# Kernel tuning notes

Measured on AMD Instinct MI355X. Metric: run time of the kernel, lower is better.

Reference implementation:

```python
import jax, jax.numpy as jnp
import numpy as np

DIM = 256
N_EMBED = 1024


def setup_inputs() -> dict:
    key = jax.random.key(0)
    k1, k2, k3 = jax.random.split(key, 3)
    input_hr = jax.random.normal(k1, (8, 64, 64, DIM), dtype=jnp.float32)
    input_lr = jax.random.normal(k2, (8, 64, 64, DIM), dtype=jnp.float32)
    # original init: uniform_(-1/n_embed, -1/n_embed) is a constant; use small uniform noise
    # around it so argmin is non-degenerate while staying faithful in scale.
    embed_lr = -1.0 / N_EMBED + 0.01 * jax.random.uniform(k3, (DIM, N_EMBED), dtype=jnp.float32)
    return {"input_hr": input_hr, "input_lr": input_lr, "embed_lr": embed_lr}


def _nearest(flat, embed):
    # flat: [N, D], embed: [D, K]
    dist = (flat ** 2).sum(1, keepdims=True) - 2.0 * flat @ embed + (embed ** 2).sum(0, keepdims=True)  # [N, K]
    ind = jnp.argmax(-dist, axis=1)  # [N]
    quant = embed.T[ind]  # [N, D]  (== F.embedding(ind, embed.T))
    return dist, ind, quant


def reference(input_hr, input_lr, embed_lr):
    shp = input_hr.shape
    flat_hr = input_hr.reshape(-1, DIM)
    flat_lr = input_lr.reshape(-1, DIM)

    # LC and HC paths use the identical codebook (embed_lr) in the original module,
    # so the distances/indices/quantized values are numerically identical; compute once.
    dist_hr, ind_hr, q_hr = _nearest(flat_hr, embed_lr)
    dist_lr, ind_lr, q_lr = _nearest(flat_lr, embed_lr)

    q_hr = q_hr.reshape(shp)
    q_lr = q_lr.reshape(shp)
    ind_hr = ind_hr.reshape(shp[:-1])
    ind_lr = ind_lr.reshape(shp[:-1])

    # eval mode (code_book_opt=False): diff = mean((quantize.detach() - input)^2)
    diff_hr = jnp.mean((jax.lax.stop_gradient(q_hr) - input_hr) ** 2)
    diff_lr = jnp.mean((jax.lax.stop_gradient(q_lr) - input_lr) ** 2)

    # straight-through estimator
    ste_hr = input_hr + jax.lax.stop_gradient(q_hr - input_hr)
    ste_lr = input_lr + jax.lax.stop_gradient(q_lr - input_lr)

    return (ste_hr, ste_lr, ste_hr, ste_lr,
            diff_hr, diff_lr, diff_hr, diff_lr,
            ind_hr, ind_lr, ind_hr, ind_lr,
            dist_hr, dist_lr, dist_hr, dist_lr)
```

## Files before the change

kernel.cpp:

```cpp
#include <hip/hip_runtime.h>
#include <stdint.h>

typedef _Float16 half8 __attribute__((ext_vector_type(8)));
typedef float f32x4 __attribute__((ext_vector_type(4)));

#define MARGIN 1e-3f

#define O_STE_HR1 0
#define O_STE_LR1 8388608
#define O_STE_HR2 16777216
#define O_STE_LR2 25165824
#define O_DIFF    33554432
#define O_IND_HR1 33554436
#define O_IND_LR1 33587204
#define O_IND_HR2 33619972
#define O_IND_LR2 33652740
#define O_DIST_HR1 33685508
#define O_DIST_LR1 67239940
#define O_DIST_HR2 100794372
#define O_DIST_LR2 134348804

#define CNT_U32_OFF 4194304

#define W_DIFF 0
#define W_CNT  16
#define W_SSE  4096
#define W_EF16 8192
#define W_ET   532480
#define W_FIND     7872512
#define W_FROWS    8134656
#define W_FMIN     8396800
#define W_T1       8658944
#define W_T3       8921088

__device__ __forceinline__ void ins2(unsigned long long k, unsigned long long &a, unsigned long long &b){
  if (k < a){ b = a; a = k; } else if (k < b){ b = k; }
}

__global__ __launch_bounds__(256) void prep(const float* __restrict__ e, char* __restrict__ ws){
  __shared__ float tile[64][65];
  int t = threadIdx.x;
  int k0 = (blockIdx.x & 3) * 64;
  int c0 = (blockIdx.x >> 2) * 64;
  float* Et = (float*)(ws + W_ET);
  _Float16* Ef = (_Float16*)(ws + W_EF16);
  float* sse = (float*)(ws + W_SSE);
#pragma unroll
  for (int p = 0; p < 4; p++){
    int kr = p*16 + (t >> 4);
    int cc = (t & 15) * 4;
    float4 v = *(const float4*)(e + (k0 + kr)*1024 + c0 + cc);
    tile[kr][cc+0]=v.x; tile[kr][cc+1]=v.y; tile[kr][cc+2]=v.z; tile[kr][cc+3]=v.w;
  }
  __syncthreads();
#pragma unroll
  for (int p = 0; p < 4; p++){
    int cr = p*16 + (t >> 4);
    int kc = (t & 15) * 4;
    float4 v;
    v.x = tile[kc+0][cr]; v.y = tile[kc+1][cr]; v.z = tile[kc+2][cr]; v.w = tile[kc+3][cr];
    *(float4*)(Et + (c0+cr)*256 + k0 + kc) = v;
    union { _Float16 h[4]; unsigned long long u; } pk;
    pk.h[0]=(_Float16)v.x; pk.h[1]=(_Float16)v.y; pk.h[2]=(_Float16)v.z; pk.h[3]=(_Float16)v.w;
    *(unsigned long long*)(Ef + (c0+cr)*256 + k0 + kc) = pk.u;
  }
  if (t < 64){
    float s = 0.f;
    for (int k = 0; k < 64; k++){ float v = tile[k][t]; s += v*v; }
    atomicAdd(&sse[c0 + t], s);
  }
}

__global__ __launch_bounds__(256) void t1x_np(const float* __restrict__ xhr, const float* __restrict__ xlr,
                                              char* __restrict__ ws, float* __restrict__ out){
  __shared__ float rowbuf[64][260];
  int b = blockIdx.x;
  int h = b >> 9;
  int r0 = (b & 511) * 64;
  const float* X = h ? xlr : xhr;
  _Float16* D = (_Float16*)(out + O_DIST_HR2) + (size_t)h*8388608;
  int t = threadIdx.x;
#pragma unroll
  for (int p = 0; p < 16; p++){
    int idx = p*256 + t;
    int rr = idx >> 6, cc = idx & 63;
    float4 v = *(const float4*)(X + (size_t)(r0+rr)*256 + cc*4);
    rowbuf[rr][cc*4+0]=v.x; rowbuf[rr][cc*4+1]=v.y; rowbuf[rr][cc*4+2]=v.z; rowbuf[rr][cc*4+3]=v.w;
    union { _Float16 h4[4]; unsigned long long u; } pk;
    pk.h4[0]=(_Float16)v.x; pk.h4[1]=(_Float16)v.y; pk.h4[2]=(_Float16)v.z; pk.h4[3]=(_Float16)v.w;
    *(unsigned long long*)(D + (size_t)(r0+rr)*256 + cc*4) = pk.u;
  }
  __syncthreads();
  if (t < 64){
    const float* a = &rowbuf[t][0];
    float blk[2];
#pragma unroll
    for (int p = 0; p < 2; p++){
      const float* ap = a + p*128;
      float s[16];
#pragma unroll
      for (int l = 0; l < 16; l++){
        float q0 = __fmul_rn(ap[l      ], ap[l      ]);
        float q1 = __fmul_rn(ap[l + 16 ], ap[l + 16 ]);
        float q2 = __fmul_rn(ap[l + 32 ], ap[l + 32 ]);
        float q3 = __fmul_rn(ap[l + 48 ], ap[l + 48 ]);
        float q4 = __fmul_rn(ap[l + 64 ], ap[l + 64 ]);
        float q5 = __fmul_rn(ap[l + 80 ], ap[l + 80 ]);
        float q6 = __fmul_rn(ap[l + 96 ], ap[l + 96 ]);
        float q7 = __fmul_rn(ap[l + 112], ap[l + 112]);
        s[l] = __fadd_rn(__fadd_rn(__fadd_rn(q0,q1), __fadd_rn(q2,q3)),
                         __fadd_rn(__fadd_rn(q4,q5), __fadd_rn(q6,q7)));
      }
      float u[8];
#pragma unroll
      for (int l = 0; l < 8; l++) u[l] = __fadd_rn(s[l], s[l+8]);
      float v[4];
#pragma unroll
      for (int l = 0; l < 4; l++) v[l] = __fadd_rn(u[l], u[l+4]);
      blk[p] = __fadd_rn(__fadd_rn(v[0], v[2]), __fadd_rn(v[1], v[3]));
    }
    ((float*)(ws + W_T1))[h*32768 + r0 + t] = __fadd_rn(blk[0], blk[1]);
  }
}

__global__ __launch_bounds__(256) void t3_np(const float* __restrict__ e, char* __restrict__ ws){
  int k = blockIdx.x*256 + threadIdx.x;
  float v0 = e[k];
  float acc = __fmul_rn(v0, v0);
  for (int i = 1; i < 256; i++){
    float v = e[i*1024 + k];
    acc = __fadd_rn(acc, __fmul_rn(v, v));
  }
  ((float*)(ws + W_T3))[k] = acc;
}

__global__ __launch_bounds__(512, 4) void gemm_dist(char* __restrict__ ws, float* __restrict__ out){
  __shared__ __align__(16) char smem[77312];
  _Float16* Bimg = (_Float16*)smem;
  float* sx = (float*)(smem + 65536);
  float* se = (float*)(smem + 66560);
  unsigned* f1tu = (unsigned*)(smem + 67072);
  unsigned* cntL = (unsigned*)(smem + 68096);
  unsigned long long* listL = (unsigned long long*)(smem + 69120);

  int bid = blockIdx.x;
  int xcd = bid & 7, slot = bid >> 3;
  int ct = slot & 7;
  int panel = ((slot >> 3) << 3) + xcd;
  int lrow0 = (panel & 127) << 8;
  int col0 = ct << 7;
  int t = threadIdx.x, lane = t & 63, wid = t >> 6;
  int wm = wid >> 1, wn = wid & 1;
  int kg = lane >> 4, rl = lane & 15;

  const _Float16* Xf = (const _Float16*)(out + O_DIST_HR2)
                     + ((panel < 128) ? 0 : 8388608) + (size_t)lrow0*256;

  const _Float16* Ef = (const _Float16*)(ws + W_EF16);
#pragma unroll
  for (int i = 0; i < 8; i++){
    int chunk = i*512 + t;
    int c = chunk >> 5, kc = chunk & 31;
    uint4 v = *(const uint4*)(Ef + (size_t)(col0 + c)*256 + kc*8);
    int off = c*512 + ((kc*16) ^ ((c & 7) << 4));
    *(uint4*)((char*)Bimg + off) = v;
  }
  if (t < 128) se[t] = ((const float*)(ws + W_SSE))[col0 + t];
  if (t < 256){
    sx[t] = ((const float*)(ws + W_T1))[((panel < 128) ? 0 : 32768) + lrow0 + t];
    f1tu[t] = 0xFFFFFFFFu;
    cntL[t] = 0u;
    listL[t*4+0] = ~0ull; listL[t*4+1] = ~0ull; listL[t*4+2] = ~0ull; listL[t*4+3] = ~0ull;
  }
  __syncthreads();

  f32x4 acc[4][4] = {};
#pragma unroll 2
  for (int kk = 0; kk < 8; kk++){
    half8 av[4], bv[4];
#pragma unroll
    for (int fm = 0; fm < 4; fm++){
      int row = wm*64 + fm*16 + rl;
      av[fm] = *(const half8*)(Xf + (size_t)row*256 + kk*32 + kg*8);
    }
#pragma unroll
    for (int fn = 0; fn < 4; fn++){
      int col = wn*64 + fn*16 + rl;
      bv[fn] = *(const half8*)((char*)Bimg + col*512 + ((kk*64 + kg*16) ^ ((col & 7) << 4)));
    }
#pragma unroll
    for (int fm = 0; fm < 4; fm++)
#pragma unroll
      for (int fn = 0; fn < 4; fn++)
        acc[fm][fn] = __builtin_amdgcn_mfma_f32_16x16x32_f16(av[fm], bv[fn], acc[fm][fn], 0, 0, 0);
  }
  __syncthreads();

  for (int fm = 0; fm < 4; fm++){
    float dmn[4] = {1e30f, 1e30f, 1e30f, 1e30f};
#pragma unroll
    for (int fn = 0; fn < 4; fn++){
      float sec = se[wn*64 + fn*16 + rl];
      f32x4 a = acc[fm][fn];
#pragma unroll
      for (int j = 0; j < 4; j++){
        int br = wm*64 + fm*16 + kg*4 + j;
        dmn[j] = fminf(dmn[j], fmaf(-2.f, a[j], sx[br] + sec));
      }
    }
#pragma unroll
    for (int m = 1; m < 16; m <<= 1)
#pragma unroll
      for (int j = 0; j < 4; j++)
        dmn[j] = fminf(dmn[j], __shfl_xor(dmn[j], m));
    if (rl == 0){
#pragma unroll
      for (int j = 0; j < 4; j++){
        int br = wm*64 + fm*16 + kg*4 + j;
        atomicMin(&f1tu[br], __float_as_uint(dmn[j]));
      }
    }
  }
  __syncthreads();

  for (int fm = 0; fm < 4; fm++){
#pragma unroll
    for (int j = 0; j < 4; j++){
      int br = wm*64 + fm*16 + kg*4 + j;
      float thrA = __uint_as_float(f1tu[br]) + MARGIN;
      float sxb = sx[br];
#pragma unroll
      for (int fn = 0; fn < 4; fn++){
        int col = wn*64 + fn*16 + rl;
        float d = fmaf(-2.f, acc[fm][fn][j], sxb + se[col]);
        *(_Float16*)(smem + br*256 + ((col*2) ^ ((br & 7) << 4))) = (_Float16)d;
        if (d <= thrA){
          unsigned idx = atomicAdd(&cntL[br], 1u);
          if (idx < 4u)
            listL[br*4 + idx] = ((unsigned long long)__float_as_uint(d) << 32) | (unsigned)(col0 + col);
        }
      }
    }
  }
  __syncthreads();

  size_t growbase = (size_t)(((panel < 128) ? 0 : 32768) + lrow0);
  char* stg = (char*)out;
#pragma unroll
  for (int it = 0; it < 16; it++){
    int idx = it*512 + t;
    int row = idx >> 5, c8 = idx & 31;
    unsigned long long v = *(const unsigned long long*)(smem + row*256 + ((c8*8) ^ ((row & 7) << 4)));
    __builtin_nontemporal_store(v,
      (unsigned long long*)(stg + (growbase + row)*2048 + col0*2 + c8*8));
  }

  if (t < 256){
    int rc = panel*256 + t;
    unsigned long long* KO = (unsigned long long*)(out + O_DIST_HR1);
    size_t kb = ((size_t)rc*8 + (size_t)ct)*4;
    KO[kb+0] = listL[t*4+0]; KO[kb+1] = listL[t*4+1];
    KO[kb+2] = listL[t*4+2]; KO[kb+3] = listL[t*4+3];
    ((unsigned*)(out + O_DIST_HR1))[CNT_U32_OFF + rc*8 + ct] = cntL[t];
  }
}

__global__ __launch_bounds__(256) void merge_flag(char* __restrict__ ws, const float* __restrict__ out){
  int rc = blockIdx.x*256 + threadIdx.x;
  const unsigned long long* K = (const unsigned long long*)(out + O_DIST_HR1);
  const unsigned* C = (const unsigned*)(out + O_DIST_HR1) + CNT_U32_OFF;
  unsigned long long a = ~0ull, b = ~0ull;
  bool ovf = false;
#pragma unroll
  for (int ct = 0; ct < 8; ct++){
    ovf = ovf || (C[(size_t)rc*8 + ct] > 4u);
    size_t base = ((size_t)rc*8 + (size_t)ct)*4;
#pragma unroll
    for (int q = 0; q < 4; q++) ins2(K[base+q], a, b);
  }
  ((int*)(ws + W_FIND))[rc] = (int)(unsigned)(a & 0xFFFFFFFFu);
  float f1 = __uint_as_float((unsigned)(a >> 32));
  float f2 = __uint_as_float((unsigned)(b >> 32));
  if (ovf || (f2 - f1 < MARGIN)){
    unsigned idx = atomicAdd((unsigned*)(ws + W_CNT), 1u);
    ((int*)(ws + W_FROWS))[idx] = rc | (ovf ? (int)0x80000000 : 0);
    ((float*)(ws + W_FMIN))[idx] = f1;
  }
}

__device__ __forceinline__ float exact_d(const float4* __restrict__ x4, const float* __restrict__ Et,
                                         float t1v, const float* __restrict__ T3, int k){
  const float4* e4 = (const float4*)(Et + (size_t)k*256);
  float c = 0.f;
  for (int i = 0; i < 64; i++){
    float4 xv = x4[i], ev = e4[i];
    c = fmaf(xv.x, ev.x, c);
    c = fmaf(xv.y, ev.y, c);
    c = fmaf(xv.z, ev.z, c);
    c = fmaf(xv.w, ev.w, c);
  }
  return __fadd_rn(__fsub_rn(t1v, __fmul_rn(2.f, c)), T3[k]);
}

__global__ __launch_bounds__(256) void refine_np(const float* __restrict__ xhr, const float* __restrict__ xlr,
                                                 char* __restrict__ ws, const float* __restrict__ out){
  unsigned nf = *(const unsigned*)(ws + W_CNT);
  int lane = threadIdx.x & 63;
  unsigned wgl = blockIdx.x*4 + (threadIdx.x >> 6);
  const float* Et = (const float*)(ws + W_ET);
  const float* T1 = (const float*)(ws + W_T1);
  const float* T3 = (const float*)(ws + W_T3);
  const int* rows = (const int*)(ws + W_FROWS);
  const float* fmn = (const float*)(ws + W_FMIN);
  int* find = (int*)(ws + W_FIND);
  const unsigned long long* K = (const unsigned long long*)(out + O_DIST_HR1);
  for (unsigned ii = wgl; ii < nf; ii += gridDim.x*4){
    int rcw = rows[ii];
    bool ovf = rcw < 0;
    int rc = rcw & 0x7FFFFFFF;
    int h = rc >> 15, r = rc & 32767;
    const float4* x4 = (const float4*)((h ? xlr : xhr) + (size_t)r*256);
    float t1v = T1[rc];
    unsigned long long bestkey = ~0ull;
    if (!ovf){
      if (lane < 32){
        unsigned long long kk = K[(size_t)rc*32 + lane];
        float dm = __uint_as_float((unsigned)(kk >> 32));
        if (dm <= fmn[ii] + MARGIN){
          int k = (int)(unsigned)(kk & 0xFFFFFFFFu);
          float d = exact_d(x4, Et, t1v, T3, k);
          bestkey = ((unsigned long long)__float_as_uint(d) << 32) | (unsigned)k;
        }
      }
    } else {
      for (int k = lane; k < 1024; k += 64){
        float d = exact_d(x4, Et, t1v, T3, k);
        unsigned long long key = ((unsigned long long)__float_as_uint(d) << 32) | (unsigned)k;
        if (key < bestkey) bestkey = key;
      }
    }
#pragma unroll
    for (int m2 = 1; m2 < 64; m2 <<= 1){
      unsigned long long o = __shfl_xor(bestkey, m2);
      if (o < bestkey) bestkey = o;
    }
    if (lane == 0) find[rc] = (int)(unsigned)(bestkey & 0xFFFFFFFFu);
  }
}

__global__ __launch_bounds__(256) void expand_dist(float* __restrict__ out){
  const unsigned long long* src = (const unsigned long long*)out;
  float* d1 = out + O_DIST_HR1;
  float* d2 = out + O_DIST_HR2;
  size_t i = (size_t)blockIdx.x*256 + threadIdx.x;
#pragma unroll
  for (int k = 0; k < 16; k++){
    size_t idx = (size_t)k*1048576 + i;
    union { unsigned long long u; _Float16 h[4]; } pk;
    pk.u = src[idx];
    f32x4 q;
    q[0] = (float)pk.h[0]; q[1] = (float)pk.h[1]; q[2] = (float)pk.h[2]; q[3] = (float)pk.h[3];
    __builtin_nontemporal_store(q, (f32x4*)(d1 + idx*4));
    __builtin_nontemporal_store(q, (f32x4*)(d2 + idx*4));
  }
}

__global__ __launch_bounds__(256) void finalize(const float* __restrict__ xhr, const float* __restrict__ xlr,
                                                char* __restrict__ ws, float* __restrict__ out){
  int b = blockIdx.x;
  int h = b >> 9, chunk = b & 511;
  const float* X = h ? xlr : xhr;
  int wid = threadIdx.x >> 6, lane = threadIdx.x & 63;
  const float* Et = (const float*)(ws + W_ET);
  const int* find = (const int*)(ws + W_FIND);
  int sb1 = h ? O_STE_LR1 : O_STE_HR1;
  int sb2 = h ? O_STE_LR2 : O_STE_HR2;
  int ib1 = h ? O_IND_LR1 : O_IND_HR1;
  int ib2 = h ? O_IND_LR2 : O_IND_HR2;
  double part = 0.0;
  for (int rr = wid; rr < 64; rr += 4){
    int r = chunk*64 + rr;
    int k = find[h*32768 + r];
    f32x4 q = *(const f32x4*)(Et + (size_t)k*256 + lane*4);
    f32x4 x = *(const f32x4*)(X + (size_t)r*256 + lane*4);
    __builtin_nontemporal_store(q, (f32x4*)(out + sb1 + r*256 + lane*4));
    __builtin_nontemporal_store(q, (f32x4*)(out + sb2 + r*256 + lane*4));
    if (lane == 0){ out[ib1 + r] = (float)k; out[ib2 + r] = (float)k; }
    double d0 = (double)q[0] - x[0], d1 = (double)q[1] - x[1];
    double d2 = (double)q[2] - x[2], d3 = (double)q[3] - x[3];
    part += d0*d0 + d1*d1 + d2*d2 + d3*d3;
  }
#pragma unroll
  for (int m = 1; m < 64; m <<= 1) part += __shfl_xor(part, m);
  __shared__ double wsum[4];
  if (lane == 0) wsum[wid] = part;
  __syncthreads();
  if (threadIdx.x == 0)
    atomicAdd((double*)(ws + W_DIFF) + h, wsum[0] + wsum[1] + wsum[2] + wsum[3]);
}

__global__ void fin_diff(const char* __restrict__ ws, float* __restrict__ out){
  if (threadIdx.x == 0 && blockIdx.x == 0){
    const double* d = (const double*)(ws + W_DIFF);
    float dh = (float)(d[0] / 8388608.0);
    float dl = (float)(d[1] / 8388608.0);
    out[O_DIFF+0] = dh; out[O_DIFF+1] = dl; out[O_DIFF+2] = dh; out[O_DIFF+3] = dl;
  }
}

extern "C" void kernel_launch(void* const* d_in, const int* in_sizes, int n_in,
                              void* d_out, int out_size, void* d_ws, size_t ws_size,
                              hipStream_t stream){
  const float* xhr = (const float*)d_in[0];
  const float* xlr = (const float*)d_in[1];
  const float* emb = (const float*)d_in[2];
  float* out = (float*)d_out;
  char* ws = (char*)d_ws;
  hipMemsetAsync(d_ws, 0, 8192, stream);
  prep<<<64, 256, 0, stream>>>(emb, ws);
  t1x_np<<<1024, 256, 0, stream>>>(xhr, xlr, ws, out);
  t3_np<<<4, 256, 0, stream>>>(emb, ws);
  gemm_dist<<<2048, 512, 0, stream>>>(ws, out);
  merge_flag<<<256, 256, 0, stream>>>(ws, out);
  refine_np<<<2048, 256, 0, stream>>>(xhr, xlr, ws, out);
  expand_dist<<<4096, 256, 0, stream>>>(out);
  finalize<<<1024, 256, 0, stream>>>(xhr, xlr, ws, out);
  fin_diff<<<1, 64, 0, stream>>>(ws, out);
}
```

Baseline: 416.7 us.

## Fuse t3 into t1x, double column tiles per GEMM block, merge refine into flag pass

The t3 codebook-norm kernel is folded into t1x as four extra blocks, which saves a launch. Each gemm_dist block now processes two column tiles in sequence, so the grid is halved and the row panel's sx load is shared between them. The merge and near-tie refinement are combined: rows in a near tie are refined per thread inside merge_refine, and only overflow rows go to a smaller refine_ovf kernel. The per-thread serial refine may diverge and run slowly when many rows are ambiguous. The halved GEMM grid also reduces parallelism.

```diff
diff --git a/kernel.cpp b/kernel.cpp
--- a/kernel.cpp
+++ b/kernel.cpp
@@ -29,7 +29,6 @@
 #define W_ET   532480
 #define W_FIND     7872512
 #define W_FROWS    8134656
-#define W_FMIN     8396800
 #define W_T1       8658944
 #define W_T3       8921088
 
@@ -72,14 +71,26 @@
 }
 
 __global__ __launch_bounds__(256) void t1x_np(const float* __restrict__ xhr, const float* __restrict__ xlr,
+                                              const float* __restrict__ e,
                                               char* __restrict__ ws, float* __restrict__ out){
+  int b = blockIdx.x;
+  int t = threadIdx.x;
+  if (b >= 1024){
+    int k = (b - 1024)*256 + t;
+    float v0 = e[k];
+    float acc = __fmul_rn(v0, v0);
+    for (int i = 1; i < 256; i++){
+      float v = e[i*1024 + k];
+      acc = __fadd_rn(acc, __fmul_rn(v, v));
+    }
+    ((float*)(ws + W_T3))[k] = acc;
+    return;
+  }
   __shared__ float rowbuf[64][260];
-  int b = blockIdx.x;
   int h = b >> 9;
   int r0 = (b & 511) * 64;
   const float* X = h ? xlr : xhr;
   _Float16* D = (_Float16*)(out + O_DIST_HR2) + (size_t)h*8388608;
-  int t = threadIdx.x;
 #pragma unroll
   for (int p = 0; p < 16; p++){
     int idx = p*256 + t;
@@ -123,17 +134,6 @@
   }
 }
 
-__global__ __launch_bounds__(256) void t3_np(const float* __restrict__ e, char* __restrict__ ws){
-  int k = blockIdx.x*256 + threadIdx.x;
-  float v0 = e[k];
-  float acc = __fmul_rn(v0, v0);
-  for (int i = 1; i < 256; i++){
-    float v = e[i*1024 + k];
-    acc = __fadd_rn(acc, __fmul_rn(v, v));
-  }
-  ((float*)(ws + W_T3))[k] = acc;
-}
-
 __global__ __launch_bounds__(512, 4) void gemm_dist(char* __restrict__ ws, float* __restrict__ out){
   __shared__ __align__(16) char smem[77312];
   _Float16* Bimg = (_Float16*)smem;
@@ -145,146 +145,130 @@
 
   int bid = blockIdx.x;
   int xcd = bid & 7, slot = bid >> 3;
-  int ct = slot & 7;
-  int panel = ((slot >> 3) << 3) + xcd;
+  int ctp = slot & 3;
+  int panel = ((slot >> 2) << 3) + xcd;
   int lrow0 = (panel & 127) << 8;
-  int col0 = ct << 7;
   int t = threadIdx.x, lane = t & 63, wid = t >> 6;
   int wm = wid >> 1, wn = wid & 1;
   int kg = lane >> 4, rl = lane & 15;
 
   const _Float16* Xf = (const _Float16*)(out + O_DIST_HR2)
                      + ((panel < 128) ? 0 : 8388608) + (size_t)lrow0*256;
-
   const _Float16* Ef = (const _Float16*)(ws + W_EF16);
-#pragma unroll
-  for (int i = 0; i < 8; i++){
-    int chunk = i*512 + t;
-    int c = chunk >> 5, kc = chunk & 31;
-    uint4 v = *(const uint4*)(Ef + (size_t)(col0 + c)*256 + kc*8);
-    int off = c*512 + ((kc*16) ^ ((c & 7) << 4));
-    *(uint4*)((char*)Bimg + off) = v;
-  }
-  if (t < 128) se[t] = ((const float*)(ws + W_SSE))[col0 + t];
-  if (t < 256){
-    sx[t] = ((const float*)(ws + W_T1))[((panel < 128) ? 0 : 32768) + lrow0 + t];
-    f1tu[t] = 0xFFFFFFFFu;
-    cntL[t] = 0u;
-    listL[t*4+0] = ~0ull; listL[t*4+1] = ~0ull; listL[t*4+2] = ~0ull; listL[t*4+3] = ~0ull;
-  }
-  __syncthreads();
-
-  f32x4 acc[4][4] = {};
+  size_t growbase = (size_t)(((panel < 128) ? 0 : 32768) + lrow0);
+  char* stg = (char*)out;
+  unsigned long long* KO = (unsigned long long*)(out + O_DIST_HR1);
+  unsigned* CO = (unsigned*)(out + O_DIST_HR1) + CNT_U32_OFF;
+
+  if (t < 256) sx[t] = ((const float*)(ws + W_T1))[((panel < 128) ? 0 : 32768) + lrow0 + t];
+
+#pragma unroll
+  for (int cti = 0; cti < 2; cti++){
+    int ct = ctp + cti*4;
+    int col0 = ct << 7;
+    __syncthreads();
+
+#pragma unroll
+    for (int i = 0; i < 8; i++){
+      int chunk = i*512 + t;
+      int c = chunk >> 5, kc = chunk & 31;
+      uint4 v = *(const uint4*)(Ef + (size_t)(col0 + c)*256 + kc*8);
+      int off = c*512 + ((kc*16) ^ ((c & 7) << 4));
+      *(uint4*)((char*)Bimg + off) = v;
+    }
+    if (t < 128) se[t] = ((const float*)(ws + W_SSE))[col0 + t];
+    if (t < 256){
+      f1tu[t] = 0xFFFFFFFFu;
+      cntL[t] = 0u;
+      listL[t*4+0] = ~0ull; listL[t*4+1] = ~0ull; listL[t*4+2] = ~0ull; listL[t*4+3] = ~0ull;
+    }
+    __syncthreads();
+
+    f32x4 acc[4][4] = {};
 #pragma unroll 2
-  for (int kk = 0; kk < 8; kk++){
-    half8 av[4], bv[4];
-#pragma unroll
+    for (int kk = 0; kk < 8; kk++){
+      half8 av[4], bv[4];
+#pragma unroll
+      for (int fm = 0; fm < 4; fm++){
+        int row = wm*64 + fm*16 + rl;
+        av[fm] = *(const half8*)(Xf + (size_t)row*256 + kk*32 + kg*8);
+      }
+#pragma unroll
+      for (int fn = 0; fn < 4; fn++){
+        int col = wn*64 + fn*16 + rl;
+        bv[fn] = *(const half8*)((char*)Bimg + col*512 + ((kk*64 + kg*16) ^ ((col & 7) << 4)));
+      }
+#pragma unroll
+      for (int fm = 0; fm < 4; fm++)
+#pragma unroll
+        for (int fn = 0; fn < 4; fn++)
+          acc[fm][fn] = __builtin_amdgcn_mfma_f32_16x16x32_f16(av[fm], bv[fn], acc[fm][fn], 0, 0, 0);
+    }
+    __syncthreads();
+
     for (int fm = 0; fm < 4; fm++){
-      int row = wm*64 + fm*16 + rl;
-      av[fm] = *(const half8*)(Xf + (size_t)row*256 + kk*32 + kg*8);
-    }
-#pragma unroll
-    for (int fn = 0; fn < 4; fn++){
-      int col = wn*64 + fn*16 + rl;
-      bv[fn] = *(const half8*)((char*)Bimg + col*512 + ((kk*64 + kg*16) ^ ((col & 7) << 4)));
-    }
-#pragma unroll
-    for (int fm = 0; fm < 4; fm++)
-#pragma unroll
-      for (int fn = 0; fn < 4; fn++)
-        acc[fm][fn] = __builtin_amdgcn_mfma_f32_16x16x32_f16(av[fm], bv[fn], acc[fm][fn], 0, 0, 0);
-  }
-  __syncthreads();
-
-  for (int fm = 0; fm < 4; fm++){
-    float dmn[4] = {1e30f, 1e30f, 1e30f, 1e30f};
-#pragma unroll
-    for (int fn = 0; fn < 4; fn++){
-      float sec = se[wn*64 + fn*16 + rl];
-      f32x4 a = acc[fm][fn];
+      float dmn[4] = {1e30f, 1e30f, 1e30f, 1e30f};
+#pragma unroll
+      for (int fn = 0; fn < 4; fn++){
+        float sec = se[wn*64 + fn*16 + rl];
+        f32x4 a = acc[fm][fn];
+#pragma unroll
+        for (int j = 0; j < 4; j++){
+          int br = wm*64 + fm*16 + kg*4 + j;
+          dmn[j] = fminf(dmn[j], fmaf(-2.f, a[j], sx[br] + sec));
+        }
+      }
+#pragma unroll
+      for (int m = 1; m < 16; m <<= 1)
+#pragma unroll
+        for (int j = 0; j < 4; j++)
+          dmn[j] = fminf(dmn[j], __shfl_xor(dmn[j], m));
+      if (rl == 0){
+#pragma unroll
+        for (int j = 0; j < 4; j++){
+          int br = wm*64 + fm*16 + kg*4 + j;
+          atomicMin(&f1tu[br], __float_as_uint(dmn[j]));
+        }
+      }
+    }
+    __syncthreads();
+
+    for (int fm = 0; fm < 4; fm++){
 #pragma unroll
       for (int j = 0; j < 4; j++){
         int br = wm*64 + fm*16 + kg*4 + j;
-        dmn[j] = fminf(dmn[j], fmaf(-2.f, a[j], sx[br] + sec));
-      }
-    }
-#pragma unroll
-    for (int m = 1; m < 16; m <<= 1)
-#pragma unroll
-      for (int j = 0; j < 4; j++)
-        dmn[j] = fminf(dmn[j], __shfl_xor(dmn[j], m));
-    if (rl == 0){
-#pragma unroll
-      for (int j = 0; j < 4; j++){
-        int br = wm*64 + fm*16 + kg*4 + j;
-        atomicMin(&f1tu[br], __float_as_uint(dmn[j]));
-      }
-    }
-  }
-  __syncthreads();
-
-  for (int fm = 0; fm < 4; fm++){
-#pragma unroll
-    for (int j = 0; j < 4; j++){
-      int br = wm*64 + fm*16 + kg*4 + j;
-      float thrA = __uint_as_float(f1tu[br]) + MARGIN;
-      float sxb = sx[br];
-#pragma unroll
-      for (int fn = 0; fn < 4; fn++){
-        int col = wn*64 + fn*16 + rl;
-        float d = fmaf(-2.f, acc[fm][fn][j], sxb + se[col]);
-        *(_Float16*)(smem + br*256 + ((col*2) ^ ((br & 7) << 4))) = (_Float16)d;
-        if (d <= thrA){
-          unsigned idx = atomicAdd(&cntL[br], 1u);
-          if (idx < 4u)
-            listL[br*4 + idx] = ((unsigned long long)__float_as_uint(d) << 32) | (unsigned)(col0 + col);
+        float thrA = __uint_as_float(f1tu[br]) + MARGIN;
+        float sxb = sx[br];
+#pragma unroll
+        for (int fn = 0; fn < 4; fn++){
+          int col = wn*64 + fn*16 + rl;
+          float d = fmaf(-2.f, acc[fm][fn][j], sxb + se[col]);
+          *(_Float16*)(smem + br*256 + ((col*2) ^ ((br & 7) << 4))) = (_Float16)d;
+          if (d <= thrA){
+            unsigned idx = atomicAdd(&cntL[br], 1u);
+            if (idx < 4u)
+              listL[br*4 + idx] = ((unsigned long long)__float_as_uint(d) << 32) | (unsigned)(col0 + col);
+          }
         }
       }
     }
-  }
-  __syncthreads();
-
-  size_t growbase = (size_t)(((panel < 128) ? 0 : 32768) + lrow0);
-  char* stg = (char*)out;
-#pragma unroll
-  for (int it = 0; it < 16; it++){
-    int idx = it*512 + t;
-    int row = idx >> 5, c8 = idx & 31;
-    unsigned long long v = *(const unsigned long long*)(smem + row*256 + ((c8*8) ^ ((row & 7) << 4)));
-    __builtin_nontemporal_store(v,
-      (unsigned long long*)(stg + (growbase + row)*2048 + col0*2 + c8*8));
-  }
-
-  if (t < 256){
-    int rc = panel*256 + t;
-    unsigned long long* KO = (unsigned long long*)(out + O_DIST_HR1);
-    size_t kb = ((size_t)rc*8 + (size_t)ct)*4;
-    KO[kb+0] = listL[t*4+0]; KO[kb+1] = listL[t*4+1];
-    KO[kb+2] = listL[t*4+2]; KO[kb+3] = listL[t*4+3];
-    ((unsigned*)(out + O_DIST_HR1))[CNT_U32_OFF + rc*8 + ct] = cntL[t];
-  }
-}
-
-__global__ __launch_bounds__(256) void merge_flag(char* __restrict__ ws, const float* __restrict__ out){
-  int rc = blockIdx.x*256 + threadIdx.x;
-  const unsigned long long* K = (const unsigned long long*)(out + O_DIST_HR1);
-  const unsigned* C = (const unsigned*)(out + O_DIST_HR1) + CNT_U32_OFF;
-  unsigned long long a = ~0ull, b = ~0ull;
-  bool ovf = false;
-#pragma unroll
-  for (int ct = 0; ct < 8; ct++){
-    ovf = ovf || (C[(size_t)rc*8 + ct] > 4u);
-    size_t base = ((size_t)rc*8 + (size_t)ct)*4;
-#pragma unroll
-    for (int q = 0; q < 4; q++) ins2(K[base+q], a, b);
-  }
-  ((int*)(ws + W_FIND))[rc] = (int)(unsigned)(a & 0xFFFFFFFFu);
-  float f1 = __uint_as_float((unsigned)(a >> 32));
-  float f2 = __uint_as_float((unsigned)(b >> 32));
-  if (ovf || (f2 - f1 < MARGIN)){
-    unsigned idx = atomicAdd((unsigned*)(ws + W_CNT), 1u);
-    ((int*)(ws + W_FROWS))[idx] = rc | (ovf ? (int)0x80000000 : 0);
-    ((float*)(ws + W_FMIN))[idx] = f1;
+    __syncthreads();
+
+#pragma unroll
+    for (int it = 0; it < 16; it++){
+      int idx = it*512 + t;
+      int row = idx >> 5, c8 = idx & 31;
+      unsigned long long v = *(const unsigned long long*)(smem + row*256 + ((c8*8) ^ ((row & 7) << 4)));
+      __builtin_nontemporal_store(v,
+        (unsigned long long*)(stg + (growbase + row)*2048 + col0*2 + c8*8));
+    }
+    if (t < 256){
+      int rc = panel*256 + t;
+      size_t kb = ((size_t)rc*8 + (size_t)ct)*4;
+      KO[kb+0] = listL[t*4+0]; KO[kb+1] = listL[t*4+1];
+      KO[kb+2] = listL[t*4+2]; KO[kb+3] = listL[t*4+3];
+      CO[rc*8 + ct] = cntL[t];
+    }
   }
 }
 
@@ -302,8 +286,49 @@
   return __fadd_rn(__fsub_rn(t1v, __fmul_rn(2.f, c)), T3[k]);
 }
 
-__global__ __launch_bounds__(256) void refine_np(const float* __restrict__ xhr, const float* __restrict__ xlr,
-                                                 char* __restrict__ ws, const float* __restrict__ out){
+__global__ __launch_bounds__(256) void merge_refine(const float* __restrict__ xhr, const float* __restrict__ xlr,
+                                                    char* __restrict__ ws, const float* __restrict__ out){
+  int rc = blockIdx.x*256 + threadIdx.x;
+  const unsigned long long* K = (const unsigned long long*)(out + O_DIST_HR1);
+  const unsigned* C = (const unsigned*)(out + O_DIST_HR1) + CNT_U32_OFF;
+  unsigned long long a = ~0ull, b = ~0ull;
+  bool ovf = false;
+#pragma unroll
+  for (int ct = 0; ct < 8; ct++){
+    ovf = ovf || (C[(size_t)rc*8 + ct] > 4u);
+    size_t base = ((size_t)rc*8 + (size_t)ct)*4;
+#pragma unroll
+    for (int q = 0; q < 4; q++) ins2(K[base+q], a, b);
+  }
+  float f1 = __uint_as_float((unsigned)(a >> 32));
+  float f2 = __uint_as_float((unsigned)(b >> 32));
+  int res = (int)(unsigned)(a & 0xFFFFFFFFu);
+  if (ovf){
+    unsigned idx = atomicAdd((unsigned*)(ws + W_CNT), 1u);
+    ((int*)(ws + W_FROWS))[idx] = rc;
+  } else if (f2 - f1 < MARGIN){
+    const float* Et = (const float*)(ws + W_ET);
+    float t1v = ((const float*)(ws + W_T1))[rc];
+    const float* T3 = (const float*)(ws + W_T3);
+    const float4* x4 = (const float4*)(((rc >= 32768) ? xlr : xhr) + (size_t)(rc & 32767)*256);
+    unsigned long long best = ~0ull;
+    for (int q = 0; q < 32; q++){
+      unsigned long long kk = K[(size_t)rc*32 + q];
+      float dm = __uint_as_float((unsigned)(kk >> 32));
+      if (dm <= f1 + MARGIN){
+        int k = (int)(unsigned)(kk & 0xFFFFFFFFu);
+        float d = exact_d(x4, Et, t1v, T3, k);
+        unsigned long long key = ((unsigned long long)__float_as_uint(d) << 32) | (unsigned)k;
+        if (key < best) best = key;
+      }
+    }
+    res = (int)(unsigned)(best & 0xFFFFFFFFu);
+  }
+  ((int*)(ws + W_FIND))[rc] = res;
+}
+
+__global__ __launch_bounds__(256) void refine_ovf(const float* __restrict__ xhr, const float* __restrict__ xlr,
+                                                  char* __restrict__ ws){
   unsigned nf = *(const unsigned*)(ws + W_CNT);
   int lane = threadIdx.x & 63;
   unsigned wgl = blockIdx.x*4 + (threadIdx.x >> 6);
@@ -311,33 +336,17 @@
   const float* T1 = (const float*)(ws + W_T1);
   const float* T3 = (const float*)(ws + W_T3);
   const int* rows = (const int*)(ws + W_FROWS);
-  const float* fmn = (const float*)(ws + W_FMIN);
   int* find = (int*)(ws + W_FIND);
-  const unsigned long long* K = (const unsigned long long*)(out + O_DIST_HR1);
   for (unsigned ii = wgl; ii < nf; ii += gridDim.x*4){
-    int rcw = rows[ii];
-    bool ovf = rcw < 0;
-    int rc = rcw & 0x7FFFFFFF;
+    int rc = rows[ii];
     int h = rc >> 15, r = rc & 32767;
     const float4* x4 = (const float4*)((h ? xlr : xhr) + (size_t)r*256);
     float t1v = T1[rc];
     unsigned long long bestkey = ~0ull;
-    if (!ovf){
-      if (lane < 32){
-        unsigned long long kk = K[(size_t)rc*32 + lane];
-        float dm = __uint_as_float((unsigned)(kk >> 32));
-        if (dm <= fmn[ii] + MARGIN){
-          int k = (int)(unsigned)(kk & 0xFFFFFFFFu);
-          float d = exact_d(x4, Et, t1v, T3, k);
-          bestkey = ((unsigned long long)__float_as_uint(d) << 32) | (unsigned)k;
-        }
-      }
-    } else {
-      for (int k = lane; k < 1024; k += 64){
-        float d = exact_d(x4, Et, t1v, T3, k);
-        unsigned long long key = ((unsigned long long)__float_as_uint(d) << 32) | (unsigned)k;
-        if (key < bestkey) bestkey = key;
-      }
+    for (int k = lane; k < 1024; k += 64){
+      float d = exact_d(x4, Et, t1v, T3, k);
+      unsigned long long key = ((unsigned long long)__float_as_uint(d) << 32) | (unsigned)k;
+      if (key < bestkey) bestkey = key;
     }
 #pragma unroll
     for (int m2 = 1; m2 < 64; m2 <<= 1){
@@ -418,11 +427,10 @@
   char* ws = (char*)d_ws;
   hipMemsetAsync(d_ws, 0, 8192, stream);
   prep<<<64, 256, 0, stream>>>(emb, ws);
-  t1x_np<<<1024, 256, 0, stream>>>(xhr, xlr, ws, out);
-  t3_np<<<4, 256, 0, stream>>>(emb, ws);
-  gemm_dist<<<2048, 512, 0, stream>>>(ws, out);
-  merge_flag<<<256, 256, 0, stream>>>(ws, out);
-  refine_np<<<2048, 256, 0, stream>>>(xhr, xlr, ws, out);
+  t1x_np<<<1028, 256, 0, stream>>>(xhr, xlr, emb, ws, out);
+  gemm_dist<<<1024, 512, 0, stream>>>(ws, out);
+  merge_refine<<<256, 256, 0, stream>>>(xhr, xlr, ws, out);
+  refine_ovf<<<64, 256, 0, stream>>>(xhr, xlr, ws);
   expand_dist<<<4096, 256, 0, stream>>>(out);
   finalize<<<1024, 256, 0, stream>>>(xhr, xlr, ws, out);
   fin_diff<<<1, 64, 0, stream>>>(ws, out);
```

Result: slower. 644.8 us (+54.7%).
